# Optimization experiments

Measured on AMD Instinct MI355X. Metric: run time of the kernel, lower is better.

## Reference

```python
import jax, jax.numpy as jnp
import numpy as np

B, L, C, D, H, NB, K = 8, 1024, 4, 64, 8, 2, 16  # batch, seq, conds, dim, heads, blocks, rbf centers

def _ln(x, s, b):
    m = x.mean(-1, keepdims=True)
    v = x.var(-1, keepdims=True)
    return (x - m) / jnp.sqrt(v + 1e-6) * s + b

def setup_inputs() -> dict:
    key = jax.random.key(0)
    ks = jax.random.split(key, 24)
    rn = lambda i, shape, sc=0.02: jax.random.normal(ks[i], shape, jnp.float32) * sc
    inp = {}
    inp['z'] = jax.random.normal(ks[0], (B, L), jnp.float32)
    inp['conditionals'] = jax.random.normal(ks[1], (C,), jnp.float32)
    inp['s'] = jnp.sort(jax.random.uniform(ks[2], (L,), jnp.float32))
    inp['embed'] = rn(3, (L, 2 * D - (C + 1)))  # positional id embedding table
    # input MLP([4D, D]) with gelu
    inp['Win1'] = rn(4, (2 * D, 4 * D)); inp['bin1'] = jnp.zeros((4 * D,), jnp.float32)
    inp['Win2'] = rn(5, (4 * D, D));     inp['bin2'] = jnp.zeros((D,), jnp.float32)
    # per-block (leading dim NB) transformer params
    inp['ln1_s'] = jnp.ones((NB, D), jnp.float32); inp['ln1_b'] = jnp.zeros((NB, D), jnp.float32)
    inp['ln2_s'] = jnp.ones((NB, D), jnp.float32); inp['ln2_b'] = jnp.zeros((NB, D), jnp.float32)
    inp['Wq'] = rn(6, (NB, D, 2 * D)); inp['bq'] = jnp.zeros((NB, 2 * D), jnp.float32)
    inp['Wk'] = rn(7, (NB, D, 2 * D)); inp['bk'] = jnp.zeros((NB, 2 * D), jnp.float32)
    inp['Wv'] = rn(8, (NB, D, 2 * D)); inp['bv'] = jnp.zeros((NB, 2 * D), jnp.float32)
    inp['Wo'] = rn(9, (NB, 2 * D, D)); inp['bo'] = jnp.zeros((NB, D), jnp.float32)
    # RBF-network attention bias: features exp(-(d-c)^2/(2w^2)) -> linear to H heads
    inp['rbf_c'] = jnp.tile(jnp.linspace(-1.0, 1.0, K, dtype=jnp.float32)[None], (NB, 1))
    inp['rbf_logw'] = jnp.full((NB, K), -1.0, jnp.float32)
    inp['rbf_w'] = rn(10, (NB, K, H), 0.1); inp['rbf_b'] = jnp.zeros((NB, H), jnp.float32)
    # FFN MLP([4D, D])
    inp['W1'] = rn(11, (NB, D, 4 * D)); inp['b1'] = jnp.zeros((NB, 4 * D), jnp.float32)
    inp['W2'] = rn(12, (NB, 4 * D, D)); inp['b2'] = jnp.zeros((NB, D), jnp.float32)
    # head MLP([4D, D, 1])
    inp['Wh1'] = rn(13, (D, 4 * D)); inp['bh1'] = jnp.zeros((4 * D,), jnp.float32)
    inp['Wh2'] = rn(14, (4 * D, D)); inp['bh2'] = jnp.zeros((D,), jnp.float32)
    inp['Wh3'] = rn(15, (D, 1));     inp['bh3'] = jnp.zeros((1,), jnp.float32)
    return inp

def reference(z, conditionals, s, embed, Win1, bin1, Win2, bin2,
              ln1_s, ln1_b, ln2_s, ln2_b, Wq, bq, Wk, bk, Wv, bv, Wo, bo,
              rbf_c, rbf_logw, rbf_w, rbf_b, W1, b1, W2, b2,
              Wh1, bh1, Wh2, bh2, Wh3, bh3):
    Bn, Ln = z.shape
    Cn = conditionals.shape[0]
    Hn = rbf_w.shape[-1]
    dh = Wq.shape[-1] // Hn
    scale = 1.0 / jnp.sqrt(jnp.float32(dh))
    # cond_as_feats: [z, broadcast conditionals] -> (B, L, C+1); prepend ids embedding -> (B, L, 2D)
    feats = jnp.concatenate([
        jnp.broadcast_to(embed[None], (Bn,) + embed.shape),
        z[..., None],
        jnp.broadcast_to(conditionals[None, None, :], (Bn, Ln, Cn)),
    ], axis=-1)
    x = jax.nn.gelu(feats @ Win1 + bin1) @ Win2 + bin2  # (B, L, D)
    dist = s[:, None] - s[None, :]  # (L, L) pairwise query-key coordinate diff (same per batch)
    for i in range(Wq.shape[0]):
        h = _ln(x, ln1_s[i], ln1_b[i])
        q = (h @ Wq[i] + bq[i]).reshape(Bn, Ln, Hn, dh)
        k = (h @ Wk[i] + bk[i]).reshape(Bn, Ln, Hn, dh)
        v = (h @ Wv[i] + bv[i]).reshape(Bn, Ln, Hn, dh)
        scores = jnp.einsum('bqhd,bkhd->bhqk', q, k) * scale
        # RBF-network bias on pairwise distances, per head
        phi = jnp.exp(-(dist[..., None] - rbf_c[i]) ** 2 / (2.0 * jnp.exp(rbf_logw[i]) ** 2))  # (L, L, K)
        bias = jnp.einsum('qkf,fh->hqk', phi, rbf_w[i]) + rbf_b[i][:, None, None]  # (H, L, L)
        a = jax.nn.softmax(scores + bias[None], axis=-1)
        o = jnp.einsum('bhqk,bkhd->bqhd', a, v).reshape(Bn, Ln, Hn * dh)
        x = x + o @ Wo[i] + bo[i]
        h2 = _ln(x, ln2_s[i], ln2_b[i])
        x = x + jax.nn.gelu(h2 @ W1[i] + b1[i]) @ W2[i] + b2[i]
    hh = jax.nn.gelu(x @ Wh1 + bh1)
    hh = jax.nn.gelu(hh @ Wh2 + bh2)
    return hh @ Wh3 + bh3  # f_hat: (B, L, 1)
```

## Files before the change

kernel.cpp:

```cpp
#include <hip/hip_runtime.h>
#include <hip/hip_bf16.h>

#define BB   8
#define LL   1024
#define DD   64
#define D2   128
#define D4   256
#define HH   8
#define DH   16

typedef __attribute__((ext_vector_type(8))) short short8;
typedef __attribute__((ext_vector_type(4))) float floatx4;

#define OFF_WIN1   0
#define OFF_WIN2   65536
#define OFF_LAY0   98304
#define LAY_STRIDE 131072
#define OFF_WQ     0
#define OFF_WK     16384
#define OFF_WV     32768
#define OFF_WO     49152
#define OFF_W1     65536
#define OFF_W2     98304
#define OFF_WH1    360448
#define OFF_WH2    393216

__device__ __forceinline__ float gelu_tanh(float u) {
  float t = tanhf(0.7978845608028654f * (u + 0.044715f * u * u * u));
  return 0.5f * u * (1.0f + t);
}

__device__ __forceinline__ float wave_reduce_sum(float v) {
#pragma unroll
  for (int m = 32; m >= 1; m >>= 1) v += __shfl_xor(v, m, 64);
  return v;
}

__device__ __forceinline__ unsigned short f2bf(float x) {
  unsigned u = __float_as_uint(x);
  u += 0x7fffu + ((u >> 16) & 1u);
  return (unsigned short)(u >> 16);
}

__device__ __forceinline__ float bf2f(unsigned short x) {
  return __uint_as_float(((unsigned)x) << 16);
}

__device__ __forceinline__ void split_bf(float v, unsigned short& hi,
                                         unsigned short& lo) {
  hi = f2bf(v);
  lo = f2bf(v - bf2f(hi));
}

template <int K, int KP>
__device__ __forceinline__ floatx4 mfma_tile(
    const unsigned short* Ah, const unsigned short* Al,
    const unsigned short* __restrict__ Bh, const unsigned short* __restrict__ Bl,
    int lq, int quad, floatx4 C) {
#pragma unroll
  for (int kk = 0; kk < K; kk += 32) {
    short8 ah = *(const short8*)(Ah + lq * KP + kk + quad * 8);
    short8 al = *(const short8*)(Al + lq * KP + kk + quad * 8);
    short8 bh = *(const short8*)(Bh + lq * K + kk + quad * 8);
    short8 bl = *(const short8*)(Bl + lq * K + kk + quad * 8);
    C = __builtin_amdgcn_mfma_f32_16x16x32_bf16(ah, bh, C, 0, 0, 0);
    C = __builtin_amdgcn_mfma_f32_16x16x32_bf16(al, bh, C, 0, 0, 0);
    C = __builtin_amdgcn_mfma_f32_16x16x32_bf16(ah, bl, C, 0, 0, 0);
  }
  return C;
}

struct PrepArgs {
  const float* src[16];
  int Kd[16], Nd[16], dst[16], elems[16];
};

__global__ __launch_bounds__(256) void k_prep(PrepArgs a,
                                              unsigned short* __restrict__ arena) {
  int mid = blockIdx.y;
  int e = blockIdx.x * 256 + threadIdx.x;
  int KN = a.elems[mid];
  if (e >= KN) return;
  int K = a.Kd[mid], N = a.Nd[mid];
  int n = e / K, k = e - n * K;
  float wv = a.src[mid][k * N + n];
  unsigned short hi, lo;
  split_bf(wv, hi, lo);
  arena[a.dst[mid] + e] = hi;
  arena[a.dst[mid] + KN + e] = lo;
}

__global__ __launch_bounds__(256) void k_input_mlp(
    const float* __restrict__ embed, const float* __restrict__ z,
    const float* __restrict__ cond, const unsigned short* __restrict__ arena,
    const float* __restrict__ bin1, const float* __restrict__ bin2,
    float* __restrict__ x) {
  __shared__ __align__(16) unsigned short Ah[16 * 136], Al[16 * 136];
  __shared__ __align__(16) unsigned short Hh[16 * 264], Hl[16 * 264];
  int t = threadIdx.x, w = t >> 6, lane = t & 63;
  int lq = lane & 15, quad = lane >> 4;
  int tok0 = blockIdx.x * 16;
  for (int idx = t; idx < 2048; idx += 256) {
    int tok = idx >> 7, dim = idx & 127;
    int bl = tok0 + tok, l = bl & (LL - 1);
    float v;
    if (dim < 123) v = embed[l * 123 + dim];
    else if (dim == 123) v = z[bl];
    else v = cond[dim - 124];
    unsigned short hi, lo;
    split_bf(v, hi, lo);
    Ah[tok * 136 + dim] = hi;
    Al[tok * 136 + dim] = lo;
  }
  __syncthreads();
  const unsigned short* B1h = arena + OFF_WIN1;
  const unsigned short* B1l = B1h + 32768;
#pragma unroll
  for (int j = 0; j < 4; ++j) {
    int tl = w * 4 + j, n = tl * 16 + lq;
    float bb = bin1[n];
    floatx4 C = {bb, bb, bb, bb};
    C = mfma_tile<128, 136>(Ah, Al, B1h + tl * 16 * 128, B1l + tl * 16 * 128,
                            lq, quad, C);
#pragma unroll
    for (int r = 0; r < 4; ++r) {
      float g = gelu_tanh(C[r]);
      unsigned short hi, lo;
      split_bf(g, hi, lo);
      Hh[(quad * 4 + r) * 264 + n] = hi;
      Hl[(quad * 4 + r) * 264 + n] = lo;
    }
  }
  __syncthreads();
  const unsigned short* B2h = arena + OFF_WIN2;
  const unsigned short* B2l = B2h + 16384;
  {
    int n = w * 16 + lq;
    float bb = bin2[n];
    floatx4 C = {bb, bb, bb, bb};
    C = mfma_tile<256, 264>(Hh, Hl, B2h + w * 16 * 256, B2l + w * 16 * 256,
                            lq, quad, C);
#pragma unroll
    for (int r = 0; r < 4; ++r)
      x[(size_t)(tok0 + quad * 4 + r) * 64 + n] = C[r];
  }
}

__global__ __launch_bounds__(256) void k_bias(
    const float* __restrict__ s, const float* __restrict__ rbf_c,
    const float* __restrict__ rbf_logw, const float* __restrict__ rbf_w,
    const float* __restrict__ rbf_b, unsigned short* __restrict__ biasT) {
  int lay = blockIdx.y;
  int id = blockIdx.x * 256 + threadIdx.x;
  int k = id >> 10, q = id & 1023;
  float dd = s[q] - s[k];
  float acc[8];
#pragma unroll
  for (int h = 0; h < 8; ++h) acc[h] = rbf_b[lay * 8 + h];
#pragma unroll 1
  for (int f = 0; f < 16; ++f) {
    float c = rbf_c[lay * 16 + f];
    float inv2w2 = 0.5f * __expf(-2.0f * rbf_logw[lay * 16 + f]);
    float e = dd - c;
    float ph = __expf(-e * e * inv2w2);
#pragma unroll
    for (int h = 0; h < 8; ++h)
      acc[h] = fmaf(ph, rbf_w[lay * 128 + f * 8 + h], acc[h]);
  }
  unsigned short* bT = biasT + (size_t)lay * 8 * 1024 * 1024;
#pragma unroll
  for (int h = 0; h < 8; ++h)
    bT[(size_t)(h * 1024 + k) * 1024 + q] = f2bf(acc[h]);
}

__global__ __launch_bounds__(256) void k_ln_qkv(
    const float* __restrict__ x, const float* __restrict__ ln_s,
    const float* __restrict__ ln_b, const unsigned short* __restrict__ arena,
    const float* __restrict__ bq, const float* __restrict__ bk,
    const float* __restrict__ bv, unsigned short* __restrict__ qo,
    unsigned short* __restrict__ ko, unsigned short* __restrict__ vo, int lay) {
  __shared__ __align__(16) unsigned short Ah[16 * 72], Al[16 * 72];
  int t = threadIdx.x, w = t >> 6, lane = t & 63;
  int tok0 = blockIdx.x * 16;
  int mat = blockIdx.y;
  float ss = ln_s[lay * 64 + lane], sb = ln_b[lay * 64 + lane];
#pragma unroll
  for (int tk = 0; tk < 4; ++tk) {
    int tok = w * 4 + tk;
    float v = x[(size_t)(tok0 + tok) * 64 + lane];
    float mean = wave_reduce_sum(v) * 0.015625f;
    float d = v - mean;
    float var = wave_reduce_sum(d * d) * 0.015625f;
    float hv = d * rsqrtf(var + 1e-6f) * ss + sb;
    unsigned short hi, lo;
    split_bf(hv, hi, lo);
    Ah[tok * 72 + lane] = hi;
    Al[tok * 72 + lane] = lo;
  }
  __syncthreads();
  int lq = lane & 15, quad = lane >> 4;
  const unsigned short* Bh =
      arena + OFF_LAY0 + lay * LAY_STRIDE + mat * 16384;
  const unsigned short* Bl = Bh + 8192;
  const float* bias = (mat == 0 ? bq : mat == 1 ? bk : bv) + lay * 128;
  unsigned short* outp = (mat == 0 ? qo : mat == 1 ? ko : vo);
  int b = tok0 >> 10, l0 = tok0 & 1023;
#pragma unroll
  for (int j = 0; j < 2; ++j) {
    int tl = w + j * 4;
    int n = tl * 16 + lq;
    float bb = bias[n];
    floatx4 C = {bb, bb, bb, bb};
    C = mfma_tile<64, 72>(Ah, Al, Bh + tl * 16 * 64, Bl + tl * 16 * 64,
                          lq, quad, C);
    size_t basea = ((size_t)(b * 8 + tl) * 1024 + l0 + quad * 4) * 16 + lq;
#pragma unroll
    for (int r = 0; r < 4; ++r)
      outp[basea + (size_t)r * 16] = f2bf(C[r]);
  }
}

__global__ __launch_bounds__(256) void k_attn(
    const unsigned short* __restrict__ qg, const unsigned short* __restrict__ kg,
    const unsigned short* __restrict__ vg, const unsigned short* __restrict__ biasT,
    float* __restrict__ og) {
  __shared__ __align__(16) unsigned short Kl[64 * 32];
  __shared__ __align__(16) unsigned short VT[16 * 72];
  __shared__ __align__(16) unsigned short Pl[4][16 * 72];
  int t = threadIdx.x, w = t >> 6, lane = t & 63;
  int lq = lane & 15, quad = lane >> 4;
  int bid = blockIdx.x;
  int b = bid >> 7, h = (bid >> 4) & 7, qblk = bid & 15;
  int q0w = qblk * 64 + w * 16;
  size_t bh = (size_t)(b * 8 + h) * 1024;

  ((uint4*)Kl)[t] = uint4{0, 0, 0, 0};

  short8 Qb = {};
  if (quad < 2)
    Qb = *(const short8*)(qg + (bh + q0w + lq) * 16 + quad * 8);

  float m = -1e30f, l = 0.0f;
  floatx4 O = {0.0f, 0.0f, 0.0f, 0.0f};

#pragma unroll 1
  for (int kc = 0; kc < 1024; kc += 64) {
    __syncthreads();
    {
      int key = t >> 2, dp = (t & 3) * 4;
      uint2 kv = *(const uint2*)(kg + (bh + kc + key) * 16 + dp);
      *(uint2*)(Kl + key * 32 + dp) = kv;
      uint2 vv = *(const uint2*)(vg + (bh + kc + key) * 16 + dp);
      VT[(dp + 0) * 72 + key] = (unsigned short)(vv.x & 0xffff);
      VT[(dp + 1) * 72 + key] = (unsigned short)(vv.x >> 16);
      VT[(dp + 2) * 72 + key] = (unsigned short)(vv.y & 0xffff);
      VT[(dp + 3) * 72 + key] = (unsigned short)(vv.y >> 16);
    }
    __syncthreads();
    float s[16];
#pragma unroll
    for (int tile = 0; tile < 4; ++tile) {
      short8 A = *(const short8*)(Kl + (tile * 16 + lq) * 32 + quad * 8);
      floatx4 c = {0.0f, 0.0f, 0.0f, 0.0f};
      c = __builtin_amdgcn_mfma_f32_16x16x32_bf16(A, Qb, c, 0, 0, 0);
      const unsigned short* bp = biasT +
          ((size_t)(h * 1024 + kc + tile * 16 + quad * 4)) * 1024 + q0w + lq;
#pragma unroll
      for (int r = 0; r < 4; ++r)
        s[tile * 4 + r] = fmaf(c[r], 0.25f, bf2f(bp[r * 1024]));
    }
    float cm = s[0];
#pragma unroll
    for (int i = 1; i < 16; ++i) cm = fmaxf(cm, s[i]);
    cm = fmaxf(cm, __shfl_xor(cm, 16, 64));
    cm = fmaxf(cm, __shfl_xor(cm, 32, 64));
    float mnew = fmaxf(m, cm);
    float alpha = __expf(m - mnew);
    float p[16], psum = 0.0f;
#pragma unroll
    for (int i = 0; i < 16; ++i) {
      p[i] = __expf(s[i] - mnew);
      psum += p[i];
    }
    psum += __shfl_xor(psum, 16, 64);
    psum += __shfl_xor(psum, 32, 64);
    l = l * alpha + psum;
    m = mnew;
    unsigned short* pw = &Pl[w][lq * 72];
#pragma unroll
    for (int tile = 0; tile < 4; ++tile) {
      uint2 pk;
      pk.x = (unsigned)f2bf(p[tile * 4 + 0]) | ((unsigned)f2bf(p[tile * 4 + 1]) << 16);
      pk.y = (unsigned)f2bf(p[tile * 4 + 2]) | ((unsigned)f2bf(p[tile * 4 + 3]) << 16);
      *(uint2*)(pw + tile * 16 + quad * 4) = pk;
    }
    asm volatile("s_waitcnt lgkmcnt(0)" ::: "memory");
#pragma unroll
    for (int r = 0; r < 4; ++r) {
      int idx = (quad * 4 + r) * 4;
      float ar = __uint_as_float(
          __builtin_amdgcn_ds_bpermute(idx, __float_as_uint(alpha)));
      O[r] *= ar;
    }
#pragma unroll
    for (int i = 0; i < 2; ++i) {
      short8 Pa = *(const short8*)(pw + i * 32 + quad * 8);
      short8 Vb = *(const short8*)(&VT[lq * 72 + i * 32 + quad * 8]);
      O = __builtin_amdgcn_mfma_f32_16x16x32_bf16(Pa, Vb, O, 0, 0, 0);
    }
  }
  float linv = 1.0f / l;
#pragma unroll
  for (int r = 0; r < 4; ++r) {
    int idx = (quad * 4 + r) * 4;
    float lr = __uint_as_float(
        __builtin_amdgcn_ds_bpermute(idx, __float_as_uint(linv)));
    og[((size_t)(b * 1024 + q0w + quad * 4 + r)) * 128 + h * 16 + lq] = O[r] * lr;
  }
}

__global__ __launch_bounds__(256) void k_proj_ffn(
    const float* __restrict__ ob, const unsigned short* __restrict__ arena,
    const float* __restrict__ bo, float* __restrict__ x,
    const float* __restrict__ ln_s, const float* __restrict__ ln_b,
    const float* __restrict__ b1, const float* __restrict__ b2, int lay) {
  __shared__ __align__(16) unsigned short Ah[16 * 136], Al[16 * 136];
  __shared__ __align__(16) unsigned short Sh[16 * 72], Sl[16 * 72];
  __shared__ __align__(16) unsigned short Hh[16 * 264], Hl[16 * 264];
  __shared__ float xl[16 * 64];
  int t = threadIdx.x, w = t >> 6, lane = t & 63;
  int lq = lane & 15, quad = lane >> 4;
  int tok0 = blockIdx.x * 16;
  const unsigned short* labase = arena + OFF_LAY0 + lay * LAY_STRIDE;
  for (int idx = t * 4; idx < 2048; idx += 1024) {
    int row = idx >> 7, col = idx & 127;
    float4 v = *(const float4*)(ob + (size_t)(tok0 + row) * 128 + col);
    unsigned short h0, e0, h1, e1, h2, e2, h3, e3;
    split_bf(v.x, h0, e0); split_bf(v.y, h1, e1);
    split_bf(v.z, h2, e2); split_bf(v.w, h3, e3);
    unsigned* ph = (unsigned*)(Ah + row * 136 + col);
    ph[0] = (unsigned)h0 | ((unsigned)h1 << 16);
    ph[1] = (unsigned)h2 | ((unsigned)h3 << 16);
    unsigned* pl = (unsigned*)(Al + row * 136 + col);
    pl[0] = (unsigned)e0 | ((unsigned)e1 << 16);
    pl[1] = (unsigned)e2 | ((unsigned)e3 << 16);
  }
  __syncthreads();
  {
    const unsigned short* Bh = labase + OFF_WO;
    const unsigned short* Bl = Bh + 8192;
    int n = w * 16 + lq;
    float bb = bo[lay * 64 + n];
    floatx4 C = {bb, bb, bb, bb};
    C = mfma_tile<128, 136>(Ah, Al, Bh + w * 16 * 128, Bl + w * 16 * 128,
                            lq, quad, C);
#pragma unroll
    for (int r = 0; r < 4; ++r) {
      int m = quad * 4 + r;
      float xv = x[(size_t)(tok0 + m) * 64 + n] + C[r];
      xl[m * 64 + n] = xv;
    }
  }
  __syncthreads();
  {
    float ss = ln_s[lay * 64 + lane], sb = ln_b[lay * 64 + lane];
#pragma unroll
    for (int tk = 0; tk < 4; ++tk) {
      int tok = w * 4 + tk;
      float v = xl[tok * 64 + lane];
      float mean = wave_reduce_sum(v) * 0.015625f;
      float d = v - mean;
      float var = wave_reduce_sum(d * d) * 0.015625f;
      float hv = d * rsqrtf(var + 1e-6f) * ss + sb;
      unsigned short hi, lo;
      split_bf(hv, hi, lo);
      Sh[tok * 72 + lane] = hi;
      Sl[tok * 72 + lane] = lo;
    }
  }
  __syncthreads();
  {
    const unsigned short* Bh = labase + OFF_W1;
    const unsigned short* Bl = Bh + 16384;
#pragma unroll
    for (int j = 0; j < 4; ++j) {
      int tl = w * 4 + j, n = tl * 16 + lq;
      float bb = b1[lay * 256 + n];
      floatx4 C = {bb, bb, bb, bb};
      C = mfma_tile<64, 72>(Sh, Sl, Bh + tl * 16 * 64, Bl + tl * 16 * 64,
                            lq, quad, C);
#pragma unroll
      for (int r = 0; r < 4; ++r) {
        float g = gelu_tanh(C[r]);
        unsigned short hi, lo;
        split_bf(g, hi, lo);
        Hh[(quad * 4 + r) * 264 + n] = hi;
        Hl[(quad * 4 + r) * 264 + n] = lo;
      }
    }
  }
  __syncthreads();
  {
    const unsigned short* Bh = labase + OFF_W2;
    const unsigned short* Bl = Bh + 16384;
    int n = w * 16 + lq;
    float bb = b2[lay * 64 + n];
    floatx4 C = {bb, bb, bb, bb};
    C = mfma_tile<256, 264>(Hh, Hl, Bh + w * 16 * 256, Bl + w * 16 * 256,
                            lq, quad, C);
#pragma unroll
    for (int r = 0; r < 4; ++r) {
      int m = quad * 4 + r;
      x[(size_t)(tok0 + m) * 64 + n] = xl[m * 64 + n] + C[r];
    }
  }
}

__global__ __launch_bounds__(256) void k_head(
    const float* __restrict__ x, const unsigned short* __restrict__ arena,
    const float* __restrict__ bh1, const float* __restrict__ bh2,
    const float* __restrict__ Wh3, const float* __restrict__ bh3,
    float* __restrict__ out) {
  __shared__ __align__(16) unsigned short Sh[16 * 72], Sl[16 * 72];
  __shared__ __align__(16) unsigned short Hh[16 * 264], Hl[16 * 264];
  __shared__ float h2s[16 * 64];
  int t = threadIdx.x, w = t >> 6, lane = t & 63;
  int lq = lane & 15, quad = lane >> 4;
  int tok0 = blockIdx.x * 16;
  {
    int idx = t * 4;
    int row = idx >> 6, col = idx & 63;
    float4 v = *(const float4*)(x + (size_t)(tok0 + row) * 64 + col);
    unsigned short h0, e0, h1, e1, h2, e2, h3, e3;
    split_bf(v.x, h0, e0); split_bf(v.y, h1, e1);
    split_bf(v.z, h2, e2); split_bf(v.w, h3, e3);
    unsigned* ph = (unsigned*)(Sh + row * 72 + col);
    ph[0] = (unsigned)h0 | ((unsigned)h1 << 16);
    ph[1] = (unsigned)h2 | ((unsigned)h3 << 16);
    unsigned* pl = (unsigned*)(Sl + row * 72 + col);
    pl[0] = (unsigned)e0 | ((unsigned)e1 << 16);
    pl[1] = (unsigned)e2 | ((unsigned)e3 << 16);
  }
  __syncthreads();
  {
    const unsigned short* Bh = arena + OFF_WH1;
    const unsigned short* Bl = Bh + 16384;
#pragma unroll
    for (int j = 0; j < 4; ++j) {
      int tl = w * 4 + j, n = tl * 16 + lq;
      float bb = bh1[n];
      floatx4 C = {bb, bb, bb, bb};
      C = mfma_tile<64, 72>(Sh, Sl, Bh + tl * 16 * 64, Bl + tl * 16 * 64,
                            lq, quad, C);
#pragma unroll
      for (int r = 0; r < 4; ++r) {
        float g = gelu_tanh(C[r]);
        unsigned short hi, lo;
        split_bf(g, hi, lo);
        Hh[(quad * 4 + r) * 264 + n] = hi;
        Hl[(quad * 4 + r) * 264 + n] = lo;
      }
    }
  }
  __syncthreads();
  {
    const unsigned short* Bh = arena + OFF_WH2;
    const unsigned short* Bl = Bh + 16384;
    int n = w * 16 + lq;
    float bb = bh2[n];
    floatx4 C = {bb, bb, bb, bb};
    C = mfma_tile<256, 264>(Hh, Hl, Bh + w * 16 * 256, Bl + w * 16 * 256,
                            lq, quad, C);
#pragma unroll
    for (int r = 0; r < 4; ++r)
      h2s[(quad * 4 + r) * 64 + n] = gelu_tanh(C[r]);
  }
  __syncthreads();
  float wv3 = Wh3[lane];
#pragma unroll
  for (int tk = 0; tk < 4; ++tk) {
    int tok = w * 4 + tk;
    float v = h2s[tok * 64 + lane] * wv3;
    float sum = wave_reduce_sum(v);
    if (lane == 0) out[tok0 + tok] = sum + bh3[0];
  }
}

extern "C" void kernel_launch(void* const* d_in, const int* in_sizes, int n_in,
                              void* d_out, int out_size, void* d_ws, size_t ws_size,
                              hipStream_t stream) {
  const float* z      = (const float*)d_in[0];
  const float* cond   = (const float*)d_in[1];
  const float* s      = (const float*)d_in[2];
  const float* embed  = (const float*)d_in[3];
  const float* Win1   = (const float*)d_in[4];
  const float* bin1   = (const float*)d_in[5];
  const float* Win2   = (const float*)d_in[6];
  const float* bin2   = (const float*)d_in[7];
  const float* ln1_s  = (const float*)d_in[8];
  const float* ln1_b  = (const float*)d_in[9];
  const float* ln2_s  = (const float*)d_in[10];
  const float* ln2_b  = (const float*)d_in[11];
  const float* Wq     = (const float*)d_in[12];
  const float* bq     = (const float*)d_in[13];
  const float* Wk     = (const float*)d_in[14];
  const float* bk     = (const float*)d_in[15];
  const float* Wv     = (const float*)d_in[16];
  const float* bv     = (const float*)d_in[17];
  const float* Wo     = (const float*)d_in[18];
  const float* bo     = (const float*)d_in[19];
  const float* rbf_c  = (const float*)d_in[20];
  const float* rbf_lw = (const float*)d_in[21];
  const float* rbf_w  = (const float*)d_in[22];
  const float* rbf_b  = (const float*)d_in[23];
  const float* W1     = (const float*)d_in[24];
  const float* b1     = (const float*)d_in[25];
  const float* W2     = (const float*)d_in[26];
  const float* b2     = (const float*)d_in[27];
  const float* Wh1    = (const float*)d_in[28];
  const float* bh1    = (const float*)d_in[29];
  const float* Wh2    = (const float*)d_in[30];
  const float* bh2    = (const float*)d_in[31];
  const float* Wh3    = (const float*)d_in[32];
  const float* bh3    = (const float*)d_in[33];

  char* base = (char*)d_ws;
  float*          x     = (float*)(base);
  unsigned short* qb    = (unsigned short*)(base + (2u << 20));
  unsigned short* kb    = (unsigned short*)(base + (4u << 20));
  unsigned short* vb    = (unsigned short*)(base + (6u << 20));
  float*          ob    = (float*)(base + (8u << 20));
  unsigned short* biasT = (unsigned short*)(base + (12u << 20));
  unsigned short* arena = (unsigned short*)(base + (48u << 20));

  PrepArgs pa;
  auto set = [&](int i, const float* sp, int K, int N, int dst) {
    pa.src[i] = sp; pa.Kd[i] = K; pa.Nd[i] = N; pa.dst[i] = dst;
    pa.elems[i] = K * N;
  };
  set(0, Win1, 128, 256, OFF_WIN1);
  set(1, Win2, 256, 64, OFF_WIN2);
  for (int lay = 0; lay < 2; ++lay) {
    int lb = OFF_LAY0 + lay * LAY_STRIDE;
    set(2 + lay * 6, Wq + lay * 8192, 64, 128, lb + OFF_WQ);
    set(3 + lay * 6, Wk + lay * 8192, 64, 128, lb + OFF_WK);
    set(4 + lay * 6, Wv + lay * 8192, 64, 128, lb + OFF_WV);
    set(5 + lay * 6, Wo + lay * 8192, 128, 64, lb + OFF_WO);
    set(6 + lay * 6, W1 + lay * 16384, 64, 256, lb + OFF_W1);
    set(7 + lay * 6, W2 + lay * 16384, 256, 64, lb + OFF_W2);
  }
  set(14, Wh1, 64, 256, OFF_WH1);
  set(15, Wh2, 256, 64, OFF_WH2);

  k_prep<<<dim3(128, 16), 256, 0, stream>>>(pa, arena);
  k_bias<<<dim3(4096, 2), 256, 0, stream>>>(s, rbf_c, rbf_lw, rbf_w, rbf_b, biasT);
  k_input_mlp<<<512, 256, 0, stream>>>(embed, z, cond, arena, bin1, bin2, x);
  for (int lay = 0; lay < 2; ++lay) {
    k_ln_qkv<<<dim3(512, 3), 256, 0, stream>>>(x, ln1_s, ln1_b, arena,
                                               bq, bk, bv, qb, kb, vb, lay);
    k_attn<<<1024, 256, 0, stream>>>(qb, kb, vb,
                                     biasT + (size_t)lay * 8 * 1024 * 1024, ob);
    k_proj_ffn<<<512, 256, 0, stream>>>(ob, arena, bo, x, ln2_s, ln2_b,
                                        b1, b2, lay);
  }
  k_head<<<512, 256, 0, stream>>>(x, arena, bh1, bh2, Wh3, bh3, (float*)d_out);
}
```

Measured before the change: 286.4 us.

## Merge bias kernel into QKV launch and prefetch K/V/bias tiles in attention

The RBF bias computation now runs as extra blocks inside the layer-0 QKV kernel instead of its own launch, saving a launch and letting the two workloads overlap. The attention kernel register-prefetches the next chunk's K, V and a 64x64 bias tile with coalesced 16-byte loads, stages the bias in shared memory, and reads it from there instead of making strided global loads per element. This costs more registers and shared memory, which may lower occupancy.

```diff
diff --git a/kernel.cpp b/kernel.cpp
--- a/kernel.cpp
+++ b/kernel.cpp
@@ -146,43 +146,47 @@
   }
 }
 
-__global__ __launch_bounds__(256) void k_bias(
-    const float* __restrict__ s, const float* __restrict__ rbf_c,
-    const float* __restrict__ rbf_logw, const float* __restrict__ rbf_w,
-    const float* __restrict__ rbf_b, unsigned short* __restrict__ biasT) {
-  int lay = blockIdx.y;
-  int id = blockIdx.x * 256 + threadIdx.x;
-  int k = id >> 10, q = id & 1023;
-  float dd = s[q] - s[k];
-  float acc[8];
-#pragma unroll
-  for (int h = 0; h < 8; ++h) acc[h] = rbf_b[lay * 8 + h];
-#pragma unroll 1
-  for (int f = 0; f < 16; ++f) {
-    float c = rbf_c[lay * 16 + f];
-    float inv2w2 = 0.5f * __expf(-2.0f * rbf_logw[lay * 16 + f]);
-    float e = dd - c;
-    float ph = __expf(-e * e * inv2w2);
-#pragma unroll
-    for (int h = 0; h < 8; ++h)
-      acc[h] = fmaf(ph, rbf_w[lay * 128 + f * 8 + h], acc[h]);
-  }
-  unsigned short* bT = biasT + (size_t)lay * 8 * 1024 * 1024;
-#pragma unroll
-  for (int h = 0; h < 8; ++h)
-    bT[(size_t)(h * 1024 + k) * 1024 + q] = f2bf(acc[h]);
-}
-
-__global__ __launch_bounds__(256) void k_ln_qkv(
+__global__ __launch_bounds__(256) void k_qkv(
     const float* __restrict__ x, const float* __restrict__ ln_s,
     const float* __restrict__ ln_b, const unsigned short* __restrict__ arena,
     const float* __restrict__ bq, const float* __restrict__ bk,
     const float* __restrict__ bv, unsigned short* __restrict__ qo,
-    unsigned short* __restrict__ ko, unsigned short* __restrict__ vo, int lay) {
+    unsigned short* __restrict__ ko, unsigned short* __restrict__ vo, int lay,
+    int bias_blocks, const float* __restrict__ s,
+    const float* __restrict__ rbf_c, const float* __restrict__ rbf_logw,
+    const float* __restrict__ rbf_w, const float* __restrict__ rbf_b,
+    unsigned short* __restrict__ biasT) {
   __shared__ __align__(16) unsigned short Ah[16 * 72], Al[16 * 72];
-  int t = threadIdx.x, w = t >> 6, lane = t & 63;
-  int tok0 = blockIdx.x * 16;
-  int mat = blockIdx.y;
+  int t = threadIdx.x;
+  int bid = blockIdx.x;
+  if (bid < bias_blocks) {
+    int blay = bid >> 12;
+    int id = (bid & 4095) * 256 + t;
+    int k = id >> 10, q = id & 1023;
+    float dd = s[q] - s[k];
+    float acc[8];
+#pragma unroll
+    for (int h = 0; h < 8; ++h) acc[h] = rbf_b[blay * 8 + h];
+#pragma unroll 1
+    for (int f = 0; f < 16; ++f) {
+      float c = rbf_c[blay * 16 + f];
+      float inv2w2 = 0.5f * __expf(-2.0f * rbf_logw[blay * 16 + f]);
+      float e = dd - c;
+      float ph = __expf(-e * e * inv2w2);
+#pragma unroll
+      for (int h = 0; h < 8; ++h)
+        acc[h] = fmaf(ph, rbf_w[blay * 128 + f * 8 + h], acc[h]);
+    }
+    unsigned short* bT = biasT + (size_t)blay * 8 * 1024 * 1024;
+#pragma unroll
+    for (int h = 0; h < 8; ++h)
+      bT[(size_t)(h * 1024 + k) * 1024 + q] = f2bf(acc[h]);
+    return;
+  }
+  int rem = bid - bias_blocks;
+  int mat = rem >> 9, blk = rem & 511;
+  int w = t >> 6, lane = t & 63;
+  int tok0 = blk * 16;
   float ss = ln_s[lay * 64 + lane], sb = ln_b[lay * 64 + lane];
 #pragma unroll
   for (int tk = 0; tk < 4; ++tk) {
@@ -199,8 +203,7 @@
   }
   __syncthreads();
   int lq = lane & 15, quad = lane >> 4;
-  const unsigned short* Bh =
-      arena + OFF_LAY0 + lay * LAY_STRIDE + mat * 16384;
+  const unsigned short* Bh = arena + OFF_LAY0 + lay * LAY_STRIDE + mat * 16384;
   const unsigned short* Bl = Bh + 8192;
   const float* bias = (mat == 0 ? bq : mat == 1 ? bk : bv) + lay * 128;
   unsigned short* outp = (mat == 0 ? qo : mat == 1 ? ko : vo);
@@ -227,6 +230,7 @@
   __shared__ __align__(16) unsigned short Kl[64 * 32];
   __shared__ __align__(16) unsigned short VT[16 * 72];
   __shared__ __align__(16) unsigned short Pl[4][16 * 72];
+  __shared__ __align__(16) unsigned short Bch[64 * 68];
   int t = threadIdx.x, w = t >> 6, lane = t & 63;
   int lq = lane & 15, quad = lane >> 4;
   int bid = blockIdx.x;
@@ -243,31 +247,54 @@
   float m = -1e30f, l = 0.0f;
   floatx4 O = {0.0f, 0.0f, 0.0f, 0.0f};
 
+  int key = t >> 2, dp = (t & 3) * 4;
+  const unsigned short* kgp = kg + (bh + key) * 16 + dp;
+  const unsigned short* vgp = vg + (bh + key) * 16 + dp;
+  int brow = t >> 3, bcol = (t & 7) * 8;
+  const unsigned short* bgp =
+      biasT + ((size_t)h * 1024) * 1024 + qblk * 64 + bcol;
+
+  uint2 kpre = *(const uint2*)(kgp);
+  uint2 vpre = *(const uint2*)(vgp);
+  uint4 bp0 = *(const uint4*)(bgp + (size_t)brow * 1024);
+  uint4 bp1 = *(const uint4*)(bgp + (size_t)(brow + 32) * 1024);
+
 #pragma unroll 1
   for (int kc = 0; kc < 1024; kc += 64) {
     __syncthreads();
+    *(uint2*)(Kl + key * 32 + dp) = kpre;
+    VT[(dp + 0) * 72 + key] = (unsigned short)(vpre.x & 0xffff);
+    VT[(dp + 1) * 72 + key] = (unsigned short)(vpre.x >> 16);
+    VT[(dp + 2) * 72 + key] = (unsigned short)(vpre.y & 0xffff);
+    VT[(dp + 3) * 72 + key] = (unsigned short)(vpre.y >> 16);
     {
-      int key = t >> 2, dp = (t & 3) * 4;
-      uint2 kv = *(const uint2*)(kg + (bh + kc + key) * 16 + dp);
-      *(uint2*)(Kl + key * 32 + dp) = kv;
-      uint2 vv = *(const uint2*)(vg + (bh + kc + key) * 16 + dp);
-      VT[(dp + 0) * 72 + key] = (unsigned short)(vv.x & 0xffff);
-      VT[(dp + 1) * 72 + key] = (unsigned short)(vv.x >> 16);
-      VT[(dp + 2) * 72 + key] = (unsigned short)(vv.y & 0xffff);
-      VT[(dp + 3) * 72 + key] = (unsigned short)(vv.y >> 16);
+      unsigned* p0 = (unsigned*)(Bch + brow * 68 + bcol);
+      p0[0] = bp0.x; p0[1] = bp0.y;
+      unsigned* p1 = (unsigned*)(Bch + brow * 68 + bcol + 4);
+      p1[0] = bp0.z; p1[1] = bp0.w;
+      unsigned* p2 = (unsigned*)(Bch + (brow + 32) * 68 + bcol);
+      p2[0] = bp1.x; p2[1] = bp1.y;
+      unsigned* p3 = (unsigned*)(Bch + (brow + 32) * 68 + bcol + 4);
+      p3[0] = bp1.z; p3[1] = bp1.w;
     }
     __syncthreads();
+    if (kc + 64 < 1024) {
+      kpre = *(const uint2*)(kgp + (size_t)(kc + 64) * 16);
+      vpre = *(const uint2*)(vgp + (size_t)(kc + 64) * 16);
+      bp0 = *(const uint4*)(bgp + (size_t)(kc + 64 + brow) * 1024);
+      bp1 = *(const uint4*)(bgp + (size_t)(kc + 64 + brow + 32) * 1024);
+    }
     float s[16];
 #pragma unroll
     for (int tile = 0; tile < 4; ++tile) {
       short8 A = *(const short8*)(Kl + (tile * 16 + lq) * 32 + quad * 8);
       floatx4 c = {0.0f, 0.0f, 0.0f, 0.0f};
       c = __builtin_amdgcn_mfma_f32_16x16x32_bf16(A, Qb, c, 0, 0, 0);
-      const unsigned short* bp = biasT +
-          ((size_t)(h * 1024 + kc + tile * 16 + quad * 4)) * 1024 + q0w + lq;
 #pragma unroll
       for (int r = 0; r < 4; ++r)
-        s[tile * 4 + r] = fmaf(c[r], 0.25f, bf2f(bp[r * 1024]));
+        s[tile * 4 + r] =
+            fmaf(c[r], 0.25f,
+                 bf2f(Bch[(tile * 16 + quad * 4 + r) * 68 + w * 16 + lq]));
     }
     float cm = s[0];
 #pragma unroll
@@ -553,11 +580,12 @@
   set(15, Wh2, 256, 64, OFF_WH2);
 
   k_prep<<<dim3(128, 16), 256, 0, stream>>>(pa, arena);
-  k_bias<<<dim3(4096, 2), 256, 0, stream>>>(s, rbf_c, rbf_lw, rbf_w, rbf_b, biasT);
   k_input_mlp<<<512, 256, 0, stream>>>(embed, z, cond, arena, bin1, bin2, x);
   for (int lay = 0; lay < 2; ++lay) {
-    k_ln_qkv<<<dim3(512, 3), 256, 0, stream>>>(x, ln1_s, ln1_b, arena,
-                                               bq, bk, bv, qb, kb, vb, lay);
+    int bias_blocks = (lay == 0) ? 8192 : 0;
+    k_qkv<<<bias_blocks + 1536, 256, 0, stream>>>(
+        x, ln1_s, ln1_b, arena, bq, bk, bv, qb, kb, vb, lay,
+        bias_blocks, s, rbf_c, rbf_lw, rbf_w, rbf_b, biasT);
     k_attn<<<1024, 256, 0, stream>>>(qb, kb, vb,
                                      biasT + (size_t)lay * 8 * 1024 * 1024, ob);
     k_proj_ffn<<<512, 256, 0, stream>>>(ob, arena, bo, x, ln2_s, ln2_b,
```

Measured after the change: 281.3 us. No clear change (-1.8%).

## Fuse QKV projection into neighbor kernels and stage bias/V tiles with prefetch

Applied to the files above, without the earlier changes.

Fuses the LN+QKV projection into the input MLP and the proj/FFN kernels, and folds the head MLP into the last FFN kernel, cutting the launch count and the x round-trips through global memory. V is now written pre-transposed, and the bias is stored row-major per query so attention can load contiguous 64x64 bias tiles into LDS with vector loads. The next K/V/bias chunk is prefetched into registers during compute. The cost is more LDS per block, heavier fused kernels with fewer independent blocks per stage, and serialized QKV matmuls within each block.

```diff
diff --git a/kernel.cpp b/kernel.cpp
--- a/kernel.cpp
+++ b/kernel.cpp
@@ -90,13 +90,102 @@
   arena[a.dst[mid] + KN + e] = lo;
 }
 
-__global__ __launch_bounds__(256) void k_input_mlp(
+__global__ __launch_bounds__(256) void k_bias(
+    const float* __restrict__ s, const float* __restrict__ rbf_c,
+    const float* __restrict__ rbf_logw, const float* __restrict__ rbf_w,
+    const float* __restrict__ rbf_b, unsigned short* __restrict__ biasT) {
+  int lay = blockIdx.y;
+  int id = blockIdx.x * 256 + threadIdx.x;
+  int q = id >> 10, k = id & 1023;
+  float dd = s[q] - s[k];
+  float acc[8];
+#pragma unroll
+  for (int h = 0; h < 8; ++h) acc[h] = rbf_b[lay * 8 + h];
+#pragma unroll 1
+  for (int f = 0; f < 16; ++f) {
+    float c = rbf_c[lay * 16 + f];
+    float inv2w2 = 0.5f * __expf(-2.0f * rbf_logw[lay * 16 + f]);
+    float e = dd - c;
+    float ph = __expf(-e * e * inv2w2);
+#pragma unroll
+    for (int h = 0; h < 8; ++h)
+      acc[h] = fmaf(ph, rbf_w[lay * 128 + f * 8 + h], acc[h]);
+  }
+  unsigned short* bT = biasT + (size_t)lay * 8 * 1024 * 1024;
+#pragma unroll
+  for (int h = 0; h < 8; ++h)
+    bT[(size_t)(h * 1024 + q) * 1024 + k] = f2bf(acc[h]);
+}
+
+__device__ __forceinline__ void qkv_tail(
+    const float* xl, unsigned short* Sh, unsigned short* Sl,
+    const unsigned short* __restrict__ arena, int lay,
+    const float* __restrict__ ln_s, const float* __restrict__ ln_b,
+    const float* __restrict__ bq, const float* __restrict__ bk,
+    const float* __restrict__ bv, unsigned short* __restrict__ qo,
+    unsigned short* __restrict__ ko, unsigned short* __restrict__ voT,
+    int tok0, int t) {
+  int w = t >> 6, lane = t & 63;
+  int lq = lane & 15, quad = lane >> 4;
+  float ss = ln_s[lay * 64 + lane], sb = ln_b[lay * 64 + lane];
+#pragma unroll
+  for (int tk = 0; tk < 4; ++tk) {
+    int tok = w * 4 + tk;
+    float v = xl[tok * 64 + lane];
+    float mean = wave_reduce_sum(v) * 0.015625f;
+    float d = v - mean;
+    float var = wave_reduce_sum(d * d) * 0.015625f;
+    float hv = d * rsqrtf(var + 1e-6f) * ss + sb;
+    unsigned short hi, lo;
+    split_bf(hv, hi, lo);
+    Sh[tok * 72 + lane] = hi;
+    Sl[tok * 72 + lane] = lo;
+  }
+  __syncthreads();
+  int b = tok0 >> 10, l0 = tok0 & 1023;
+#pragma unroll 1
+  for (int mat = 0; mat < 3; ++mat) {
+    const unsigned short* Bh =
+        arena + OFF_LAY0 + lay * LAY_STRIDE + mat * 16384;
+    const unsigned short* Bl = Bh + 8192;
+    const float* bias = (mat == 0 ? bq : mat == 1 ? bk : bv) + lay * 128;
+#pragma unroll
+    for (int j = 0; j < 2; ++j) {
+      int tl = w + j * 4;
+      int n = tl * 16 + lq;
+      float bb = bias[n];
+      floatx4 C = {bb, bb, bb, bb};
+      C = mfma_tile<64, 72>(Sh, Sl, Bh + tl * 16 * 64, Bl + tl * 16 * 64,
+                            lq, quad, C);
+      if (mat < 2) {
+        unsigned short* outp = (mat == 0 ? qo : ko);
+        size_t basea = ((size_t)(b * 8 + tl) * 1024 + l0 + quad * 4) * 16 + lq;
+#pragma unroll
+        for (int r = 0; r < 4; ++r)
+          outp[basea + (size_t)r * 16] = f2bf(C[r]);
+      } else {
+        size_t basev = ((size_t)(b * 8 + tl) * 16 + lq) * 1024 + l0 + quad * 4;
+#pragma unroll
+        for (int r = 0; r < 4; ++r)
+          voT[basev + r] = f2bf(C[r]);
+      }
+    }
+  }
+}
+
+__global__ __launch_bounds__(256) void k_in_qkv(
     const float* __restrict__ embed, const float* __restrict__ z,
     const float* __restrict__ cond, const unsigned short* __restrict__ arena,
     const float* __restrict__ bin1, const float* __restrict__ bin2,
-    float* __restrict__ x) {
+    float* __restrict__ x, const float* __restrict__ ln1_s,
+    const float* __restrict__ ln1_b, const float* __restrict__ bq,
+    const float* __restrict__ bk, const float* __restrict__ bv,
+    unsigned short* __restrict__ qo, unsigned short* __restrict__ ko,
+    unsigned short* __restrict__ voT) {
   __shared__ __align__(16) unsigned short Ah[16 * 136], Al[16 * 136];
   __shared__ __align__(16) unsigned short Hh[16 * 264], Hl[16 * 264];
+  __shared__ __align__(16) unsigned short Sh[16 * 72], Sl[16 * 72];
+  __shared__ float xl[16 * 64];
   int t = threadIdx.x, w = t >> 6, lane = t & 63;
   int lq = lane & 15, quad = lane >> 4;
   int tok0 = blockIdx.x * 16;
@@ -141,98 +230,32 @@
     C = mfma_tile<256, 264>(Hh, Hl, B2h + w * 16 * 256, B2l + w * 16 * 256,
                             lq, quad, C);
 #pragma unroll
-    for (int r = 0; r < 4; ++r)
-      x[(size_t)(tok0 + quad * 4 + r) * 64 + n] = C[r];
-  }
-}
-
-__global__ __launch_bounds__(256) void k_bias(
-    const float* __restrict__ s, const float* __restrict__ rbf_c,
-    const float* __restrict__ rbf_logw, const float* __restrict__ rbf_w,
-    const float* __restrict__ rbf_b, unsigned short* __restrict__ biasT) {
-  int lay = blockIdx.y;
-  int id = blockIdx.x * 256 + threadIdx.x;
-  int k = id >> 10, q = id & 1023;
-  float dd = s[q] - s[k];
-  float acc[8];
-#pragma unroll
-  for (int h = 0; h < 8; ++h) acc[h] = rbf_b[lay * 8 + h];
-#pragma unroll 1
-  for (int f = 0; f < 16; ++f) {
-    float c = rbf_c[lay * 16 + f];
-    float inv2w2 = 0.5f * __expf(-2.0f * rbf_logw[lay * 16 + f]);
-    float e = dd - c;
-    float ph = __expf(-e * e * inv2w2);
-#pragma unroll
-    for (int h = 0; h < 8; ++h)
-      acc[h] = fmaf(ph, rbf_w[lay * 128 + f * 8 + h], acc[h]);
-  }
-  unsigned short* bT = biasT + (size_t)lay * 8 * 1024 * 1024;
-#pragma unroll
-  for (int h = 0; h < 8; ++h)
-    bT[(size_t)(h * 1024 + k) * 1024 + q] = f2bf(acc[h]);
-}
-
-__global__ __launch_bounds__(256) void k_ln_qkv(
-    const float* __restrict__ x, const float* __restrict__ ln_s,
-    const float* __restrict__ ln_b, const unsigned short* __restrict__ arena,
-    const float* __restrict__ bq, const float* __restrict__ bk,
-    const float* __restrict__ bv, unsigned short* __restrict__ qo,
-    unsigned short* __restrict__ ko, unsigned short* __restrict__ vo, int lay) {
-  __shared__ __align__(16) unsigned short Ah[16 * 72], Al[16 * 72];
-  int t = threadIdx.x, w = t >> 6, lane = t & 63;
-  int tok0 = blockIdx.x * 16;
-  int mat = blockIdx.y;
-  float ss = ln_s[lay * 64 + lane], sb = ln_b[lay * 64 + lane];
-#pragma unroll
-  for (int tk = 0; tk < 4; ++tk) {
-    int tok = w * 4 + tk;
-    float v = x[(size_t)(tok0 + tok) * 64 + lane];
-    float mean = wave_reduce_sum(v) * 0.015625f;
-    float d = v - mean;
-    float var = wave_reduce_sum(d * d) * 0.015625f;
-    float hv = d * rsqrtf(var + 1e-6f) * ss + sb;
-    unsigned short hi, lo;
-    split_bf(hv, hi, lo);
-    Ah[tok * 72 + lane] = hi;
-    Al[tok * 72 + lane] = lo;
-  }
-  __syncthreads();
-  int lq = lane & 15, quad = lane >> 4;
-  const unsigned short* Bh =
-      arena + OFF_LAY0 + lay * LAY_STRIDE + mat * 16384;
-  const unsigned short* Bl = Bh + 8192;
-  const float* bias = (mat == 0 ? bq : mat == 1 ? bk : bv) + lay * 128;
-  unsigned short* outp = (mat == 0 ? qo : mat == 1 ? ko : vo);
-  int b = tok0 >> 10, l0 = tok0 & 1023;
-#pragma unroll
-  for (int j = 0; j < 2; ++j) {
-    int tl = w + j * 4;
-    int n = tl * 16 + lq;
-    float bb = bias[n];
-    floatx4 C = {bb, bb, bb, bb};
-    C = mfma_tile<64, 72>(Ah, Al, Bh + tl * 16 * 64, Bl + tl * 16 * 64,
-                          lq, quad, C);
-    size_t basea = ((size_t)(b * 8 + tl) * 1024 + l0 + quad * 4) * 16 + lq;
-#pragma unroll
-    for (int r = 0; r < 4; ++r)
-      outp[basea + (size_t)r * 16] = f2bf(C[r]);
-  }
+    for (int r = 0; r < 4; ++r) {
+      int m = quad * 4 + r;
+      x[(size_t)(tok0 + m) * 64 + n] = C[r];
+      xl[m * 64 + n] = C[r];
+    }
+  }
+  __syncthreads();
+  qkv_tail(xl, Sh, Sl, arena, 0, ln1_s, ln1_b, bq, bk, bv,
+           qo, ko, voT, tok0, t);
 }
 
 __global__ __launch_bounds__(256) void k_attn(
     const unsigned short* __restrict__ qg, const unsigned short* __restrict__ kg,
-    const unsigned short* __restrict__ vg, const unsigned short* __restrict__ biasT,
+    const unsigned short* __restrict__ vgT, const unsigned short* __restrict__ biasT,
     float* __restrict__ og) {
   __shared__ __align__(16) unsigned short Kl[64 * 32];
   __shared__ __align__(16) unsigned short VT[16 * 72];
   __shared__ __align__(16) unsigned short Pl[4][16 * 72];
+  __shared__ __align__(16) unsigned short Bch[64 * 72];
   int t = threadIdx.x, w = t >> 6, lane = t & 63;
   int lq = lane & 15, quad = lane >> 4;
   int bid = blockIdx.x;
   int b = bid >> 7, h = (bid >> 4) & 7, qblk = bid & 15;
   int q0w = qblk * 64 + w * 16;
   size_t bh = (size_t)(b * 8 + h) * 1024;
+  size_t bh16 = (size_t)(b * 8 + h) * 16;
 
   ((uint4*)Kl)[t] = uint4{0, 0, 0, 0};
 
@@ -243,31 +266,45 @@
   float m = -1e30f, l = 0.0f;
   floatx4 O = {0.0f, 0.0f, 0.0f, 0.0f};
 
+  int key = t >> 2, dp = (t & 3) * 4;
+  int drow = t >> 4, vcol = (t & 15) * 4;
+  int qrow = t >> 2, bcol = (t & 3) * 16;
+  const unsigned short* kgp = kg + (bh + key) * 16 + dp;
+  const unsigned short* vgp = vgT + (bh16 + drow) * 1024 + vcol;
+  const unsigned short* bgp =
+      biasT + ((size_t)(h * 1024 + qblk * 64 + qrow)) * 1024 + bcol;
+
+  uint2 kpre = *(const uint2*)(kgp);
+  uint2 vpre = *(const uint2*)(vgp);
+  uint4 bpre0 = *(const uint4*)(bgp);
+  uint4 bpre1 = *(const uint4*)(bgp + 8);
+
 #pragma unroll 1
   for (int kc = 0; kc < 1024; kc += 64) {
     __syncthreads();
-    {
-      int key = t >> 2, dp = (t & 3) * 4;
-      uint2 kv = *(const uint2*)(kg + (bh + kc + key) * 16 + dp);
-      *(uint2*)(Kl + key * 32 + dp) = kv;
-      uint2 vv = *(const uint2*)(vg + (bh + kc + key) * 16 + dp);
-      VT[(dp + 0) * 72 + key] = (unsigned short)(vv.x & 0xffff);
-      VT[(dp + 1) * 72 + key] = (unsigned short)(vv.x >> 16);
-      VT[(dp + 2) * 72 + key] = (unsigned short)(vv.y & 0xffff);
-      VT[(dp + 3) * 72 + key] = (unsigned short)(vv.y >> 16);
-    }
+    *(uint2*)(Kl + key * 32 + dp) = kpre;
+    *(uint2*)(VT + drow * 72 + vcol) = vpre;
+    *(uint4*)(Bch + qrow * 72 + bcol) = bpre0;
+    *(uint4*)(Bch + qrow * 72 + bcol + 8) = bpre1;
     __syncthreads();
+    if (kc + 64 < 1024) {
+      kpre = *(const uint2*)(kgp + (size_t)(kc + 64) * 16);
+      vpre = *(const uint2*)(vgp + (kc + 64));
+      bpre0 = *(const uint4*)(bgp + (kc + 64));
+      bpre1 = *(const uint4*)(bgp + (kc + 64) + 8);
+    }
     float s[16];
 #pragma unroll
     for (int tile = 0; tile < 4; ++tile) {
       short8 A = *(const short8*)(Kl + (tile * 16 + lq) * 32 + quad * 8);
       floatx4 c = {0.0f, 0.0f, 0.0f, 0.0f};
       c = __builtin_amdgcn_mfma_f32_16x16x32_bf16(A, Qb, c, 0, 0, 0);
-      const unsigned short* bp = biasT +
-          ((size_t)(h * 1024 + kc + tile * 16 + quad * 4)) * 1024 + q0w + lq;
-#pragma unroll
-      for (int r = 0; r < 4; ++r)
-        s[tile * 4 + r] = fmaf(c[r], 0.25f, bf2f(bp[r * 1024]));
+      ushort4 bb = *(const ushort4*)(Bch + (w * 16 + lq) * 72 +
+                                     tile * 16 + quad * 4);
+      s[tile * 4 + 0] = fmaf(c[0], 0.25f, bf2f(bb.x));
+      s[tile * 4 + 1] = fmaf(c[1], 0.25f, bf2f(bb.y));
+      s[tile * 4 + 2] = fmaf(c[2], 0.25f, bf2f(bb.z));
+      s[tile * 4 + 3] = fmaf(c[3], 0.25f, bf2f(bb.w));
     }
     float cm = s[0];
 #pragma unroll
@@ -319,18 +356,16 @@
   }
 }
 
-__global__ __launch_bounds__(256) void k_proj_ffn(
+__device__ __forceinline__ void pf_body(
     const float* __restrict__ ob, const unsigned short* __restrict__ arena,
     const float* __restrict__ bo, float* __restrict__ x,
     const float* __restrict__ ln_s, const float* __restrict__ ln_b,
-    const float* __restrict__ b1, const float* __restrict__ b2, int lay) {
-  __shared__ __align__(16) unsigned short Ah[16 * 136], Al[16 * 136];
-  __shared__ __align__(16) unsigned short Sh[16 * 72], Sl[16 * 72];
-  __shared__ __align__(16) unsigned short Hh[16 * 264], Hl[16 * 264];
-  __shared__ float xl[16 * 64];
-  int t = threadIdx.x, w = t >> 6, lane = t & 63;
+    const float* __restrict__ b1, const float* __restrict__ b2, int lay,
+    unsigned short* Ah, unsigned short* Al, unsigned short* Sh,
+    unsigned short* Sl, unsigned short* Hh, unsigned short* Hl, float* xl,
+    int tok0, int t, bool write_x) {
+  int w = t >> 6, lane = t & 63;
   int lq = lane & 15, quad = lane >> 4;
-  int tok0 = blockIdx.x * 16;
   const unsigned short* labase = arena + OFF_LAY0 + lay * LAY_STRIDE;
   for (int idx = t * 4; idx < 2048; idx += 1024) {
     int row = idx >> 7, col = idx & 127;
@@ -357,8 +392,7 @@
 #pragma unroll
     for (int r = 0; r < 4; ++r) {
       int m = quad * 4 + r;
-      float xv = x[(size_t)(tok0 + m) * 64 + n] + C[r];
-      xl[m * 64 + n] = xv;
+      xl[m * 64 + n] = x[(size_t)(tok0 + m) * 64 + n] + C[r];
     }
   }
   __syncthreads();
@@ -411,35 +445,59 @@
 #pragma unroll
     for (int r = 0; r < 4; ++r) {
       int m = quad * 4 + r;
-      x[(size_t)(tok0 + m) * 64 + n] = xl[m * 64 + n] + C[r];
-    }
-  }
-}
-
-__global__ __launch_bounds__(256) void k_head(
-    const float* __restrict__ x, const unsigned short* __restrict__ arena,
+      float xv = xl[m * 64 + n] + C[r];
+      xl[m * 64 + n] = xv;
+      if (write_x) x[(size_t)(tok0 + m) * 64 + n] = xv;
+    }
+  }
+  __syncthreads();
+}
+
+__global__ __launch_bounds__(256) void k_pf_qkv(
+    const float* __restrict__ ob, const unsigned short* __restrict__ arena,
+    const float* __restrict__ bo, float* __restrict__ x,
+    const float* __restrict__ ln2_s, const float* __restrict__ ln2_b,
+    const float* __restrict__ b1, const float* __restrict__ b2, int lay,
+    const float* __restrict__ ln1_s, const float* __restrict__ ln1_b,
+    const float* __restrict__ bq, const float* __restrict__ bk,
+    const float* __restrict__ bv, unsigned short* __restrict__ qo,
+    unsigned short* __restrict__ ko, unsigned short* __restrict__ voT) {
+  __shared__ __align__(16) unsigned short Ah[16 * 136], Al[16 * 136];
+  __shared__ __align__(16) unsigned short Sh[16 * 72], Sl[16 * 72];
+  __shared__ __align__(16) unsigned short Hh[16 * 264], Hl[16 * 264];
+  __shared__ float xl[16 * 64];
+  int t = threadIdx.x;
+  int tok0 = blockIdx.x * 16;
+  pf_body(ob, arena, bo, x, ln2_s, ln2_b, b1, b2, lay,
+          Ah, Al, Sh, Sl, Hh, Hl, xl, tok0, t, true);
+  qkv_tail(xl, Sh, Sl, arena, lay + 1, ln1_s, ln1_b, bq, bk, bv,
+           qo, ko, voT, tok0, t);
+}
+
+__global__ __launch_bounds__(256) void k_pf_head(
+    const float* __restrict__ ob, const unsigned short* __restrict__ arena,
+    const float* __restrict__ bo, float* __restrict__ x,
+    const float* __restrict__ ln2_s, const float* __restrict__ ln2_b,
+    const float* __restrict__ b1, const float* __restrict__ b2, int lay,
     const float* __restrict__ bh1, const float* __restrict__ bh2,
     const float* __restrict__ Wh3, const float* __restrict__ bh3,
     float* __restrict__ out) {
+  __shared__ __align__(16) unsigned short Ah[16 * 136], Al[16 * 136];
   __shared__ __align__(16) unsigned short Sh[16 * 72], Sl[16 * 72];
   __shared__ __align__(16) unsigned short Hh[16 * 264], Hl[16 * 264];
-  __shared__ float h2s[16 * 64];
+  __shared__ float xl[16 * 64];
   int t = threadIdx.x, w = t >> 6, lane = t & 63;
   int lq = lane & 15, quad = lane >> 4;
   int tok0 = blockIdx.x * 16;
-  {
-    int idx = t * 4;
-    int row = idx >> 6, col = idx & 63;
-    float4 v = *(const float4*)(x + (size_t)(tok0 + row) * 64 + col);
-    unsigned short h0, e0, h1, e1, h2, e2, h3, e3;
-    split_bf(v.x, h0, e0); split_bf(v.y, h1, e1);
-    split_bf(v.z, h2, e2); split_bf(v.w, h3, e3);
-    unsigned* ph = (unsigned*)(Sh + row * 72 + col);
-    ph[0] = (unsigned)h0 | ((unsigned)h1 << 16);
-    ph[1] = (unsigned)h2 | ((unsigned)h3 << 16);
-    unsigned* pl = (unsigned*)(Sl + row * 72 + col);
-    pl[0] = (unsigned)e0 | ((unsigned)e1 << 16);
-    pl[1] = (unsigned)e2 | ((unsigned)e3 << 16);
+  pf_body(ob, arena, bo, x, ln2_s, ln2_b, b1, b2, lay,
+          Ah, Al, Sh, Sl, Hh, Hl, xl, tok0, t, false);
+#pragma unroll
+  for (int tk = 0; tk < 4; ++tk) {
+    int tok = w * 4 + tk;
+    unsigned short hi, lo;
+    split_bf(xl[tok * 64 + lane], hi, lo);
+    Sh[tok * 72 + lane] = hi;
+    Sl[tok * 72 + lane] = lo;
   }
   __syncthreads();
   {
@@ -471,16 +529,17 @@
     floatx4 C = {bb, bb, bb, bb};
     C = mfma_tile<256, 264>(Hh, Hl, Bh + w * 16 * 256, Bl + w * 16 * 256,
                             lq, quad, C);
+    __syncthreads();
 #pragma unroll
     for (int r = 0; r < 4; ++r)
-      h2s[(quad * 4 + r) * 64 + n] = gelu_tanh(C[r]);
+      xl[(quad * 4 + r) * 64 + n] = gelu_tanh(C[r]);
   }
   __syncthreads();
   float wv3 = Wh3[lane];
 #pragma unroll
   for (int tk = 0; tk < 4; ++tk) {
     int tok = w * 4 + tk;
-    float v = h2s[tok * 64 + lane] * wv3;
+    float v = xl[tok * 64 + lane] * wv3;
     float sum = wave_reduce_sum(v);
     if (lane == 0) out[tok0 + tok] = sum + bh3[0];
   }
@@ -528,7 +587,7 @@
   float*          x     = (float*)(base);
   unsigned short* qb    = (unsigned short*)(base + (2u << 20));
   unsigned short* kb    = (unsigned short*)(base + (4u << 20));
-  unsigned short* vb    = (unsigned short*)(base + (6u << 20));
+  unsigned short* vbT   = (unsigned short*)(base + (6u << 20));
   float*          ob    = (float*)(base + (8u << 20));
   unsigned short* biasT = (unsigned short*)(base + (12u << 20));
   unsigned short* arena = (unsigned short*)(base + (48u << 20));
@@ -554,14 +613,13 @@
 
   k_prep<<<dim3(128, 16), 256, 0, stream>>>(pa, arena);
   k_bias<<<dim3(4096, 2), 256, 0, stream>>>(s, rbf_c, rbf_lw, rbf_w, rbf_b, biasT);
-  k_input_mlp<<<512, 256, 0, stream>>>(embed, z, cond, arena, bin1, bin2, x);
-  for (int lay = 0; lay < 2; ++lay) {
-    k_ln_qkv<<<dim3(512, 3), 256, 0, stream>>>(x, ln1_s, ln1_b, arena,
-                                               bq, bk, bv, qb, kb, vb, lay);
-    k_attn<<<1024, 256, 0, stream>>>(qb, kb, vb,
-                                     biasT + (size_t)lay * 8 * 1024 * 1024, ob);
-    k_proj_ffn<<<512, 256, 0, stream>>>(ob, arena, bo, x, ln2_s, ln2_b,
-                                        b1, b2, lay);
-  }
-  k_head<<<512, 256, 0, stream>>>(x, arena, bh1, bh2, Wh3, bh3, (float*)d_out);
-}
+  k_in_qkv<<<512, 256, 0, stream>>>(embed, z, cond, arena, bin1, bin2, x,
+                                    ln1_s, ln1_b, bq, bk, bv, qb, kb, vbT);
+  k_attn<<<1024, 256, 0, stream>>>(qb, kb, vbT, biasT, ob);
+  k_pf_qkv<<<512, 256, 0, stream>>>(ob, arena, bo, x, ln2_s, ln2_b, b1, b2, 0,
+                                    ln1_s, ln1_b, bq, bk, bv, qb, kb, vbT);
+  k_attn<<<1024, 256, 0, stream>>>(qb, kb, vbT,
+                                   biasT + (size_t)8 * 1024 * 1024, ob);
+  k_pf_head<<<512, 256, 0, stream>>>(ob, arena, bo, x, ln2_s, ln2_b, b1, b2, 1,
+                                     bh1, bh2, Wh3, bh3, (float*)d_out);
+}
```

Result: faster. 275.4 us (-3.8%).
